# Performance work log

Hardware: AMD Instinct MI355X
Metric: run time of the kernel (lower is better)

## Reference

```python
import jax, jax.numpy as jnp
import numpy as np

N = 64      # SSM state size (hidden_size)
H = 1024    # channels
L = 2048    # sequence length
BATCH = 8


def setup_inputs() -> dict:
    key = jax.random.key(0)
    ks = jax.random.split(key, 12)
    s = 1.0 / np.sqrt(N)
    n = jnp.arange(N, dtype=jnp.float32)
    return {
        "r": jax.random.normal(ks[0], (BATCH, L, H), dtype=jnp.float32),
        "B_re": jax.random.normal(ks[1], (N,), dtype=jnp.float32) * s,
        "B_im": jax.random.normal(ks[2], (N,), dtype=jnp.float32) * s,
        "C_re": jax.random.normal(ks[3], (H, N), dtype=jnp.float32) * s,
        "C_im": jax.random.normal(ks[4], (H, N), dtype=jnp.float32) * s,
        "P_re": jax.random.normal(ks[5], (N,), dtype=jnp.float32) * s,
        "P_im": jax.random.normal(ks[6], (N,), dtype=jnp.float32) * s,
        "Q_re": jax.random.normal(ks[7], (N,), dtype=jnp.float32) * s,
        "Q_im": jax.random.normal(ks[8], (N,), dtype=jnp.float32) * s,
        # HiPPO-LegS-like diagonal: negative real part for stability, imag ~ pi*n
        "diag_re": -0.5 * jnp.ones((N,), dtype=jnp.float32),
        "diag_im": jnp.pi * (n - N / 2.0),
        "step": jnp.array([1e-3], dtype=jnp.float32),
        "D": jnp.zeros((1,), dtype=jnp.float32),
    }


def _dplr_kernel(Bc, Cc, Pc, Qc, Lam, step, seq_len):
    # Standard S4 DPLR generating function evaluated at roots of unity,
    # then inverse FFT -> real convolution kernel K_c of shape (H, L).
    z = jnp.exp(-2j * jnp.pi * jnp.arange(seq_len) / seq_len).astype(jnp.complex64)  # (L,)
    g = (2.0 / step) * (1.0 - z) / (1.0 + z)                                          # (L,)
    cden = 1.0 / (g[:, None] - Lam[None, :])                                          # (L,N) Cauchy denom
    k00 = jnp.einsum('hn,ln->hl', Cc * Bc, cden)   # (H,L)
    k01 = jnp.einsum('hn,ln->hl', Cc * Pc, cden)   # (H,L)
    k10 = jnp.einsum('n,ln->l', Qc * Bc, cden)     # (L,)
    k11 = jnp.einsum('n,ln->l', Qc * Pc, cden)     # (L,)
    at_roots = (2.0 / (1.0 + z)) * (k00 - k01 * (k10 / (1.0 + k11)))  # (H,L)
    return jnp.fft.ifft(at_roots, axis=-1).real


def reference(r, B_re, B_im, C_re, C_im, P_re, P_im, Q_re, Q_im,
              diag_re, diag_im, step, D):
    step_c = jnp.maximum(step[0], 1e-6)
    Bc = B_re + 1j * B_im
    Cc = C_re + 1j * C_im
    Pc = P_re + 1j * P_im
    Qc = Q_re + 1j * Q_im
    Lam = diag_re + 1j * diag_im
    seq_len = r.shape[1]
    K = _dplr_kernel(Bc, Cc, Pc, Qc, Lam, step_c, seq_len)  # (H, L)
    # causal FFT convolution along the sequence axis
    nfft = 2 * seq_len
    Kf = jnp.fft.rfft(K, n=nfft, axis=-1)            # (H, nfft//2+1)
    uf = jnp.fft.rfft(r, n=nfft, axis=1)             # (B, nfft//2+1, H)
    h1 = jnp.fft.irfft(uf * Kf.T[None], n=nfft, axis=1)[:, :seq_len]  # (B,L,H)
    y1 = h1 + D[0] * r
    return jax.nn.gelu(y1, approximate=False)
```

## Files before the change

### kernel.cpp

```cpp
#include <hip/hip_runtime.h>
#include <math.h>

#define SSM_N 64
#define SSM_H 1024
#define SSM_L 2048
#define SSM_B 8
#define FFTN 2048
#define NT 256

#define PSWZ(a) ((a) ^ (((a) >> 4) & 15))

typedef float f2 __attribute__((ext_vector_type(2)));
static __device__ __forceinline__ f2 mkf2(float a, float b){ f2 v; v.x = a; v.y = b; return v; }

static __device__ __forceinline__ f2 cmul(f2 a, f2 b){
  return mkf2(-a.y, a.y) * mkf2(b.y, b.x) + mkf2(a.x, a.x) * b;
}
static __device__ __forceinline__ f2 cconj(f2 a){ return mkf2(a.x, -a.y); }

template<bool INV> static __device__ __forceinline__ f2 mul_mi(f2 a){
  return INV ? mkf2(-a.y, a.x) : mkf2(a.y, -a.x);
}
template<bool INV> static __device__ __forceinline__ f2 mul_w81(f2 a){
  const float r = 0.70710678118654752440f;
  return INV ? (r * mkf2(a.x - a.y, a.y + a.x)) : (r * mkf2(a.x + a.y, a.y - a.x));
}
template<bool INV> static __device__ __forceinline__ f2 mul_w83(f2 a){
  const float r = 0.70710678118654752440f;
  return INV ? (r * mkf2(-(a.x + a.y), a.x - a.y)) : (r * mkf2(a.y - a.x, -(a.x + a.y)));
}

#define W8C0 1.f
#define W8S0 0.f
#define W8C1 0.92387953251f
#define W8S1 (-0.38268343236f)
#define W8C2 0.70710678119f
#define W8S2 (-0.70710678119f)
#define W8C3 0.38268343236f
#define W8S3 (-0.92387953251f)
#define W8C4 0.f
#define W8S4 (-1.f)
#define W8C5 (-0.38268343236f)
#define W8S5 (-0.92387953251f)
#define W8C6 (-0.70710678119f)
#define W8S6 (-0.70710678119f)
#define W8C7 (-0.92387953251f)
#define W8S7 (-0.38268343236f)

template<bool INV>
static __device__ __forceinline__ void bfly8(const f2* x, f2* y)
{
  f2 t0=x[0]+x[4], t4=x[0]-x[4];
  f2 t1=x[1]+x[5], t5=x[1]-x[5];
  f2 t2=x[2]+x[6], t6=x[2]-x[6];
  f2 t3=x[3]+x[7], t7=x[3]-x[7];
  f2 b0=t0+t2, b2=t0-t2, b1=t1+t3, b3=t1-t3;
  f2 mb3 = mul_mi<INV>(b3);
  y[0]=b0+b1; y[4]=b0-b1; y[2]=b2+mb3; y[6]=b2-mb3;
  f2 v1 = mul_w81<INV>(t5), v2 = mul_mi<INV>(t6), v3 = mul_w83<INV>(t7);
  f2 a0=t4+v2, a2=t4-v2, a1=v1+v3, a3=v1-v3;
  f2 ma3 = mul_mi<INV>(a3);
  y[1]=a0+a1; y[5]=a0-a1; y[3]=a2+ma3; y[7]=a2-ma3;
}

template<bool INV>
static __device__ __forceinline__ void calc_w8(const f2* __restrict__ tw, int j, f2* w)
{
  f2 w1 = tw[j];
  if (INV) w1.y = -w1.y;
  w[1]=w1; w[2]=cmul(w1,w1); w[3]=cmul(w[2],w1); w[4]=cmul(w[2],w[2]);
  w[5]=cmul(w[3],w[2]); w[6]=cmul(w[3],w[3]); w[7]=cmul(w[4],w[3]);
}

static __device__ __forceinline__ void twstore(f2* __restrict__ dst, const f2* y, const f2* w,
                                               int base, int S)
{
  dst[PSWZ(base)]     = y[0];
  dst[PSWZ(base+S)]   = cmul(y[1],w[1]);
  dst[PSWZ(base+2*S)] = cmul(y[2],w[2]);
  dst[PSWZ(base+3*S)] = cmul(y[3],w[3]);
  dst[PSWZ(base+4*S)] = cmul(y[4],w[4]);
  dst[PSWZ(base+5*S)] = cmul(y[5],w[5]);
  dst[PSWZ(base+6*S)] = cmul(y[6],w[6]);
  dst[PSWZ(base+7*S)] = cmul(y[7],w[7]);
}

template<bool INV>
static __device__ __forceinline__ void bfly8_store(f2* __restrict__ dst, const f2* __restrict__ tw,
                                                   f2* x, int j, int base, int S)
{
  f2 y[8]; bfly8<INV>(x, y);
  f2 w[8]; calc_w8<INV>(tw, j, w);
  twstore(dst, y, w, base, S);
}

template<bool INV, int S>
static __device__ __forceinline__ void stage8_mid(const f2* __restrict__ src, f2* __restrict__ dst,
                                                  const f2* __restrict__ tw, int t, int st)
{
  const f2* sp = src + st;
  f2 x[8];
  #pragma unroll
  for (int q = 0; q < 8; ++q) x[q] = sp[256*q];
  int i = t & (S-1);
  int j = t - i;
  bfly8_store<INV>(dst, tw, x, j, i + j*8, S);
}

template<bool INV, int S>
static __device__ __forceinline__ void stage8_mid2(const f2* __restrict__ s0, f2* __restrict__ d0,
                                                   const f2* __restrict__ s1, f2* __restrict__ d1,
                                                   const f2* __restrict__ tw, int t, int st)
{
  f2 x0[8], x1[8];
  #pragma unroll
  for (int q = 0; q < 8; ++q) x0[q] = s0[st + 256*q];
  #pragma unroll
  for (int q = 0; q < 8; ++q) x1[q] = s1[st + 256*q];
  int i = t & (S-1), j = t - i, base = i + j*8;
  f2 w[8]; calc_w8<INV>(tw, j, w);
  f2 y[8];
  bfly8<INV>(x0, y); twstore(d0, y, w, base, S);
  bfly8<INV>(x1, y); twstore(d1, y, w, base, S);
}

template<bool INV, bool HALFOUT>
static __device__ __forceinline__ void stage4f(const f2* __restrict__ src, f2* __restrict__ dst, int st)
{
  #pragma unroll
  for (int hh = 0; hh < 2; ++hh) {
    const f2* sp = src + st + 256*hh;
    f2* wp = dst + st + 256*hh;
    f2 x0=sp[0], x1=sp[512], x2=sp[1024], x3=sp[1536];
    f2 a0=x0+x2, a2=x0-x2, a1=x1+x3, a3=x1-x3;
    f2 m = mul_mi<INV>(a3);
    wp[0]   = a0+a1;
    wp[512] = a2+m;
    if (!HALFOUT) {
      wp[1024] = a0-a1;
      wp[1536] = a2-m;
    }
  }
}

template<bool INV>
static __device__ __forceinline__ void stage4f_reg(const f2* __restrict__ src, f2* out, int st)
{
  #pragma unroll
  for (int hh = 0; hh < 2; ++hh) {
    const f2* sp = src + st + 256*hh;
    f2 x0=sp[0], x1=sp[512], x2=sp[1024], x3=sp[1536];
    f2 a0=x0+x2, a2=x0-x2, a1=x1+x3, a3=x1-x3;
    f2 m = mul_mi<INV>(a3);
    out[hh]   = a0+a1;
    out[hh+2] = a2+m;
    out[hh+4] = a0-a1;
    out[hh+6] = a2-m;
  }
}

static __device__ __forceinline__ f2 init_tw(f2* tw, int t)
{
  float s, c;
  sincosf(-6.2831853071795864769f * (float)t / (float)FFTN, &s, &c);
  f2 v = mkf2(c, s);
  tw[t] = v;
  return v;
}

__global__ __launch_bounds__(256) void kprep(
    const float* __restrict__ r, float* __restrict__ rT,
    const float* __restrict__ B_re, const float* __restrict__ B_im,
    const float* __restrict__ P_re, const float* __restrict__ P_im,
    const float* __restrict__ Q_re, const float* __restrict__ Q_im,
    const float* __restrict__ diag_re, const float* __restrict__ diag_im,
    const float* __restrict__ step,
    f2* __restrict__ cdenT, f2* __restrict__ f2v, f2* __restrict__ facv)
{
  __shared__ float til[64][65];
  int bid = blockIdx.x;
  int t = threadIdx.x;
  if (bid < 4096) {
    int tx = t & 15, ty = t >> 4;
    int h0 = (bid & 15) * 64, l0 = ((bid >> 4) & 31) * 64, b = bid >> 9;
    const float4* s4 = (const float4*)(r + ((size_t)b*SSM_L + l0)*SSM_H + h0);
    #pragma unroll
    for (int i = 0; i < 4; ++i) {
      int lr = ty + 16*i;
      float4 v = s4[(size_t)lr*(SSM_H/4) + tx];
      til[lr][4*tx+0]=v.x; til[lr][4*tx+1]=v.y; til[lr][4*tx+2]=v.z; til[lr][4*tx+3]=v.w;
    }
    __syncthreads();
    float4* d4 = (float4*)(rT + ((size_t)b*SSM_H + h0)*SSM_L + l0);
    #pragma unroll
    for (int i = 0; i < 4; ++i) {
      int hr = ty + 16*i;
      float4 w;
      w.x = til[4*tx+0][hr]; w.y = til[4*tx+1][hr];
      w.z = til[4*tx+2][hr]; w.w = til[4*tx+3][hr];
      d4[(size_t)hr*(SSM_L/4) + tx] = w;
    }
  } else {
    int gid = (bid - 4096) * 256 + t;
    int l = gid >> 3, s = gid & 7;
    double stepc = (double)step[0]; if (stepc < 1e-6) stepc = 1e-6;
    double ang = -2.0 * 3.14159265358979323846 * (double)l / (double)SSM_L;
    double zr = cos(ang), zi = sin(ang);
    double dr = 1.0 + zr, di = zi;
    double nr = 1.0 - zr, ni = -zi;
    double den = dr*dr + di*di;
    double i2s = 2.0 / stepc;
    double gr = i2s * (nr*dr + ni*di) / den;
    double gi = i2s * (ni*dr - nr*di) / den;
    double k10r=0.0, k10i=0.0, k11r=0.0, k11i=0.0;
    #pragma unroll
    for (int q = 0; q < 8; ++q) {
      int n = s*8 + q;
      double ar = gr - (double)diag_re[n];
      double ai = gi - (double)diag_im[n];
      double d2 = ar*ar + ai*ai;
      double cr = ar/d2, ci = -ai/d2;
      cdenT[n*SSM_L + l] = mkf2((float)cr, (float)ci);
      double qr = (double)Q_re[n], qi = (double)Q_im[n];
      double br = (double)B_re[n], bi = (double)B_im[n];
      double pr = (double)P_re[n], pi = (double)P_im[n];
      double qbr = qr*br - qi*bi, qbi = qr*bi + qi*br;
      double qpr = qr*pr - qi*pi, qpi = qr*pi + qi*pr;
      k10r += qbr*cr - qbi*ci; k10i += qbr*ci + qbi*cr;
      k11r += qpr*cr - qpi*ci; k11i += qpr*ci + qpi*cr;
    }
    #pragma unroll
    for (int off = 1; off < 8; off <<= 1) {
      k10r += __shfl_xor(k10r, off);
      k10i += __shfl_xor(k10i, off);
      k11r += __shfl_xor(k11r, off);
      k11i += __shfl_xor(k11i, off);
    }
    if (s == 0) {
      f2v[l] = mkf2((float)(2.0*dr/den), (float)(-2.0*di/den));
      double er = 1.0 + k11r, ei = k11i;
      double ed = er*er + ei*ei;
      facv[l] = mkf2((float)((k10r*er + k10i*ei)/ed), (float)((k10i*er - k10r*ei)/ed));
    }
  }
}

__global__ __launch_bounds__(NT, 2) void kkern(
    const float* __restrict__ C_re, const float* __restrict__ C_im,
    const float* __restrict__ B_re, const float* __restrict__ B_im,
    const float* __restrict__ P_re, const float* __restrict__ P_im,
    const f2* __restrict__ cdenT, const f2* __restrict__ f2v, const f2* __restrict__ facv,
    float4* __restrict__ PQg)
{
  __shared__ f2 bufA[2][FFTN];
  __shared__ f2 bufB[2][FFTN];
  __shared__ f2 tw[256];
  int t = threadIdx.x, st = PSWZ(t);
  int h0 = blockIdx.x * 2;
  f2 u = init_tw(tw, t);
  f2* cbs = bufA[0];
  if (t < 128) {
    int h = h0 + (t >> 6), n = t & 63;
    f2 cc = mkf2(C_re[h*SSM_N + n], C_im[h*SSM_N + n]);
    cbs[t]       = cmul(cc, mkf2(B_re[n], B_im[n]));
    cbs[128 + t] = cmul(cc, mkf2(P_re[n], P_im[n]));
  }
  __syncthreads();
  f2 k00[2][8], k01[2][8];
  #pragma unroll
  for (int h = 0; h < 2; ++h)
    #pragma unroll
    for (int i = 0; i < 8; ++i) { k00[h][i] = mkf2(0.f,0.f); k01[h][i] = mkf2(0.f,0.f); }
  f2 cd[8];
  #pragma unroll
  for (int i = 0; i < 8; ++i) cd[i] = cdenT[t + i*NT];
  for (int n = 0; n < SSM_N; ++n) {
    f2 cdn[8];
    #pragma unroll
    for (int i = 0; i < 8; ++i) cdn[i] = cdenT[((n+1)&63)*SSM_L + t + i*NT];
    #pragma unroll
    for (int h = 0; h < 2; ++h) {
      f2 cb = cbs[h*64 + n], cp = cbs[128 + h*64 + n];
      #pragma unroll
      for (int i = 0; i < 8; ++i) {
        k00[h][i] = k00[h][i] + cmul(cb, cd[i]);
        k01[h][i] = k01[h][i] + cmul(cp, cd[i]);
      }
    }
    #pragma unroll
    for (int i = 0; i < 8; ++i) cd[i] = cdn[i];
  }
  float sb, cb2;
  sincosf(-3.14159265358979f * (float)t / (float)FFTN, &sb, &cb2);
  f2 cbase = mkf2(cb2, sb);
  __syncthreads();
  f2 ar[2][8];
  #pragma unroll
  for (int hh = 0; hh < 2; ++hh)
    #pragma unroll
    for (int i = 0; i < 8; ++i) {
      int l = t + i*NT;
      f2 fv = f2v[l], fc = facv[l];
      ar[hh][i] = cmul(fv, k00[hh][i] - cmul(k01[hh][i], fc));
      bufA[hh][PSWZ(l)] = ar[hh][i];
    }
  __syncthreads();
  f2 ebin[2][4], e2048[2];
  e2048[0] = mkf2(0.f,0.f); e2048[1] = mkf2(0.f,0.f);
  #pragma unroll
  for (int ch = 0; ch < 2; ++ch) {
    #pragma unroll
    for (int i = 0; i < 4; ++i) {
      int m = t + i*NT;
      if (m == 0) {
        ebin[ch][0] = mkf2(bufA[ch][0].x, 0.f);
        e2048[ch]   = mkf2(bufA[ch][PSWZ(FFTN/2)].x, 0.f);
      } else {
        ebin[ch][i] = 0.5f * (bufA[ch][PSWZ(m)] + cconj(bufA[ch][PSWZ(FFTN - m)]));
      }
    }
  }
  {
    f2 w[8]; calc_w8<true>(tw, t, w);
    f2 y[8];
    bfly8<true>(ar[0], y); twstore(bufB[0], y, w, t*8, 1);
    bfly8<true>(ar[1], y); twstore(bufB[1], y, w, t*8, 1);
  }
  __syncthreads();
  stage8_mid2<true, 8>(bufB[0], bufA[0], bufB[1], bufA[1], tw, t, st);
  __syncthreads();
  stage8_mid2<true, 64>(bufA[0], bufB[0], bufA[1], bufB[1], tw, t, st);
  __syncthreads();
  {
    f2 kr0[8], kr1[8];
    stage4f_reg<true>(bufB[0], kr0, st);
    stage4f_reg<true>(bufB[1], kr1, st);
    const float Wc8[8] = {W8C0,W8C1,W8C2,W8C3,W8C4,W8C5,W8C6,W8C7};
    const float Ws8[8] = {W8S0,W8S1,W8S2,W8S3,W8S4,W8S5,W8S6,W8S7};
    const float scale = 1.0f / (float)FFTN;
    #pragma unroll
    for (int q = 0; q < 8; ++q) {
      f2 tq = cmul(cbase, mkf2(Wc8[q], Ws8[q]));
      kr0[q] = (kr0[q].x * scale) * tq;
      kr1[q] = (kr1[q].x * scale) * tq;
    }
    f2 w[8]; calc_w8<false>(tw, t, w);
    f2 y[8];
    bfly8<false>(kr0, y); twstore(bufA[0], y, w, t*8, 1);
    bfly8<false>(kr1, y); twstore(bufA[1], y, w, t*8, 1);
  }
  __syncthreads();
  stage8_mid2<false, 8>(bufA[0], bufB[0], bufA[1], bufB[1], tw, t, st);
  __syncthreads();
  stage8_mid2<false, 64>(bufB[0], bufA[0], bufB[1], bufA[1], tw, t, st);
  __syncthreads();
  #pragma unroll
  for (int ch = 0; ch < 2; ++ch) {
    stage4f<false, true>(bufA[ch], bufB[ch], st);
    #pragma unroll
    for (int i = 0; i < 4; ++i) {
      int m = t + i*NT;
      f2 v = ebin[ch][i];
      if (m == 0) v = e2048[ch];
      bufB[ch][1024 + m] = v;
    }
  }
  __syncthreads();
  const float q4 = 1.0f / 4096.0f;
  const f2 c1 = mkf2(0.99999882345170176f, -0.00153398018628477f);
  f2 base_odd = cmul(c1, u);
  const float Wc8[8] = {W8C0,W8C1,W8C2,W8C3,W8C4,W8C5,W8C6,W8C7};
  const float Ws8[8] = {W8S0,W8S1,W8S2,W8S3,W8S4,W8S5,W8S6,W8S7};
  #pragma unroll
  for (int ch = 0; ch < 2; ++ch) {
    float4* pqrow = PQg + (size_t)(h0 + ch) * FFTN;
    #pragma unroll
    for (int i = 0; i < 4; ++i) {
      int m = t + i*NT;
      f2 Ka = ebin[ch][i];
      f2 Kb = bufB[ch][1024 + ((1024 - m) & 1023)];
      f2 ee = cmul(u, mkf2(Wc8[2*i], Ws8[2*i]));
      float cv = ee.x, sv = -ee.y;
      float am = q4*(1.f - sv), ap = q4*(1.f + sv), cq = q4*cv;
      f2 P = mkf2(Ka.x*am + Kb.x*ap, Ka.y*am - Kb.y*ap);
      f2 dd = mkf2(Ka.x - Kb.x, Ka.y + Kb.y);
      pqrow[2*m] = make_float4(P.x, P.y, -dd.y*cq, dd.x*cq);
      f2 Ko = bufB[ch][PSWZ(m)];
      f2 Kp = bufB[ch][PSWZ(1023 - m)];
      f2 eo = cmul(base_odd, mkf2(Wc8[2*i], Ws8[2*i]));
      cv = eo.x; sv = -eo.y;
      am = q4*(1.f - sv); ap = q4*(1.f + sv); cq = q4*cv;
      f2 P2 = mkf2(Ko.x*am + Kp.x*ap, Ko.y*am - Kp.y*ap);
      f2 d2 = mkf2(Ko.x - Kp.x, Ko.y + Kp.y);
      pqrow[2*m+1] = make_float4(P2.x, P2.y, -d2.y*cq, d2.x*cq);
    }
  }
}

__global__ __launch_bounds__(NT, 4) void kconv(float* __restrict__ rT,
                                               const float4* __restrict__ PQg,
                                               const float* __restrict__ Dp)
{
  __shared__ f2 bufA[FFTN];
  __shared__ f2 bufB[FFTN];
  __shared__ f2 tw[256];
  int t = threadIdx.x, st = PSWZ(t);
  int xc = blockIdx.x & 7, y = blockIdx.x >> 3;
  int h = xc * 128 + (y >> 3);
  int b = y & 7;
  float Dv = Dp[0];
  init_tw(tw, t);
  float* rrow = rT + ((size_t)b*SSM_H + h) * SSM_L;
  const f2* r2 = (const f2*)rrow;
  f2 rv[4];
  #pragma unroll
  for (int i = 0; i < 4; ++i) rv[i] = r2[t + i*NT];
  {
    f2 xx[8];
    #pragma unroll
    for (int q = 0; q < 4; ++q) { xx[q] = rv[q]; xx[q+4] = mkf2(0.f, 0.f); }
    bfly8_store<false>(bufB, tw, xx, t, t*8, 1);
  }
  __syncthreads();
  stage8_mid<false, 8>(bufB, bufA, tw, t, st);
  __syncthreads();
  stage8_mid<false, 64>(bufA, bufB, tw, t, st);
  __syncthreads();
  const float4* pqrow = PQg + (size_t)h * FFTN;
  float4 pq[8];
  #pragma unroll
  for (int i = 0; i < 8; ++i) pq[i] = pqrow[t + i*NT];
  stage4f<false, false>(bufB, bufA, st);
  __syncthreads();
  {
    f2 xx[8];
    #pragma unroll
    for (int i = 0; i < 8; ++i) {
      int k = t + i*NT;
      int kk = (FFTN - k) & (FFTN - 1);
      f2 Ck  = bufA[st + i*NT];
      f2 Ckk = bufA[PSWZ(kk)];
      xx[i] = cmul(mkf2(pq[i].x, pq[i].y), Ck) + cmul(mkf2(pq[i].z, pq[i].w), cconj(Ckk));
    }
    bfly8_store<true>(bufB, tw, xx, t, t*8, 1);
  }
  __syncthreads();
  stage8_mid<true, 8>(bufB, bufA, tw, t, st);
  __syncthreads();
  stage8_mid<true, 64>(bufA, bufB, tw, t, st);
  __syncthreads();
  f2* o2 = (f2*)rrow;
  #pragma unroll
  for (int hh = 0; hh < 2; ++hh) {
    const f2* sp = bufB + st + 256*hh;
    f2 x0=sp[0], x1=sp[512], x2=sp[1024], x3=sp[1536];
    f2 a0=x0+x2, a2=x0-x2, a1=x1+x3, a3=x1-x3;
    f2 mm = mul_mi<true>(a3);
    f2 y0 = a0+a1, y1 = a2+mm;
    f2 rA = rv[hh], rB = rv[hh+2];
    o2[t + 256*hh]       = mkf2(y0.x + Dv*rA.x, y0.y + Dv*rA.y);
    o2[t + 256*hh + 512] = mkf2(y1.x + Dv*rB.x, y1.y + Dv*rB.y);
  }
}

__global__ __launch_bounds__(256) void ktback(const float* __restrict__ yT, float* __restrict__ out)
{
  __shared__ float til[64][65];
  int t = threadIdx.x, tx = t & 15, ty = t >> 4;
  int h0 = blockIdx.x * 64, l0 = blockIdx.y * 64, b = blockIdx.z;
  const float4* s4 = (const float4*)(yT + ((size_t)b*SSM_H + h0)*SSM_L + l0);
  #pragma unroll
  for (int i = 0; i < 4; ++i) {
    int hr = ty + 16*i;
    float4 v = s4[(size_t)hr*(SSM_L/4) + tx];
    til[hr][4*tx+0]=v.x; til[hr][4*tx+1]=v.y; til[hr][4*tx+2]=v.z; til[hr][4*tx+3]=v.w;
  }
  __syncthreads();
  float4* d4 = (float4*)(out + ((size_t)b*SSM_L + l0)*SSM_H + h0);
  #pragma unroll
  for (int i = 0; i < 4; ++i) {
    int lr = ty + 16*i;
    float4 w;
    float x0 = til[4*tx+0][lr], x1 = til[4*tx+1][lr];
    float x2 = til[4*tx+2][lr], x3 = til[4*tx+3][lr];
    w.x = 0.5f * x0 * (1.0f + erff(x0 * 0.70710678118654752f));
    w.y = 0.5f * x1 * (1.0f + erff(x1 * 0.70710678118654752f));
    w.z = 0.5f * x2 * (1.0f + erff(x2 * 0.70710678118654752f));
    w.w = 0.5f * x3 * (1.0f + erff(x3 * 0.70710678118654752f));
    d4[(size_t)lr*(SSM_H/4) + tx] = w;
  }
}

extern "C" void kernel_launch(void* const* d_in, const int* in_sizes, int n_in,
                              void* d_out, int out_size, void* d_ws, size_t ws_size,
                              hipStream_t stream)
{
  const float* r       = (const float*)d_in[0];
  const float* B_re    = (const float*)d_in[1];
  const float* B_im    = (const float*)d_in[2];
  const float* C_re    = (const float*)d_in[3];
  const float* C_im    = (const float*)d_in[4];
  const float* P_re    = (const float*)d_in[5];
  const float* P_im    = (const float*)d_in[6];
  const float* Q_re    = (const float*)d_in[7];
  const float* Q_im    = (const float*)d_in[8];
  const float* diag_re = (const float*)d_in[9];
  const float* diag_im = (const float*)d_in[10];
  const float* step    = (const float*)d_in[11];
  const float* Dp      = (const float*)d_in[12];
  float* out = (float*)d_out;

  char* p = (char*)d_ws;
  float* rT  = (float*)p;  p += (size_t)SSM_B*SSM_H*SSM_L*sizeof(float);
  f2* cdenT  = (f2*)p;     p += (size_t)SSM_N*SSM_L*sizeof(f2);
  f2* f2v    = (f2*)p;     p += (size_t)SSM_L*sizeof(f2);
  f2* facv   = (f2*)p;     p += (size_t)SSM_L*sizeof(f2);
  float4* PQ = (float4*)p; p += (size_t)SSM_H*FFTN*sizeof(float4);

  kprep<<<4096 + 64, 256, 0, stream>>>(r, rT, B_re, B_im, P_re, P_im, Q_re, Q_im,
                                       diag_re, diag_im, step, cdenT, f2v, facv);
  kkern<<<SSM_H/2, NT, 0, stream>>>(C_re, C_im, B_re, B_im, P_re, P_im,
                                    cdenT, f2v, facv, PQ);
  kconv<<<SSM_B*SSM_H, NT, 0, stream>>>(rT, PQ, Dp);
  ktback<<<dim3(SSM_H/64, SSM_L/64, SSM_B), 256, 0, stream>>>(rT, out);
}
```

Measured before the change: 265.3 us.

## Halve kconv shared memory with in-place FFT stages; widen kkern to 512 threads

kconv now runs its FFT stages in place on one shared buffer. Each stage reads into registers, syncs, then writes back, which halves LDS per block and lets launch bounds ask for 8 blocks per CU. kkern moves to 512 threads, with each half-block handling one channel's FFTs instead of one thread doing both, which cuts per-thread registers and adds parallelism. The cost is an extra barrier per in-place stage in kconv.

```diff
diff --git a/kernel.cpp b/kernel.cpp
--- a/kernel.cpp
+++ b/kernel.cpp
@@ -7,6 +7,7 @@
 #define SSM_B 8
 #define FFTN 2048
 #define NT 256
+#define NT2 512
 
 #define PSWZ(a) ((a) ^ (((a) >> 4) & 15))
 
@@ -94,6 +95,22 @@
   twstore(dst, y, w, base, S);
 }
 
+template<bool INV, bool ZTOP>
+static __device__ __forceinline__ void stage8_first(const f2* __restrict__ src, f2* __restrict__ dst,
+                                                    const f2* __restrict__ tw, int t, int st)
+{
+  const f2* sp = src + st;
+  f2 x[8];
+  if (ZTOP) {
+    #pragma unroll
+    for (int q = 0; q < 4; ++q) { x[q] = sp[256*q]; x[q+4] = mkf2(0.f, 0.f); }
+  } else {
+    #pragma unroll
+    for (int q = 0; q < 8; ++q) x[q] = sp[256*q];
+  }
+  bfly8_store<INV>(dst, tw, x, t, t*8, 1);
+}
+
 template<bool INV, int S>
 static __device__ __forceinline__ void stage8_mid(const f2* __restrict__ src, f2* __restrict__ dst,
                                                   const f2* __restrict__ tw, int t, int st)
@@ -108,20 +125,17 @@
 }
 
 template<bool INV, int S>
-static __device__ __forceinline__ void stage8_mid2(const f2* __restrict__ s0, f2* __restrict__ d0,
-                                                   const f2* __restrict__ s1, f2* __restrict__ d1,
-                                                   const f2* __restrict__ tw, int t, int st)
-{
-  f2 x0[8], x1[8];
-  #pragma unroll
-  for (int q = 0; q < 8; ++q) x0[q] = s0[st + 256*q];
-  #pragma unroll
-  for (int q = 0; q < 8; ++q) x1[q] = s1[st + 256*q];
-  int i = t & (S-1), j = t - i, base = i + j*8;
-  f2 w[8]; calc_w8<INV>(tw, j, w);
-  f2 y[8];
-  bfly8<INV>(x0, y); twstore(d0, y, w, base, S);
-  bfly8<INV>(x1, y); twstore(d1, y, w, base, S);
+static __device__ __forceinline__ void stage8_mid_ip(f2* __restrict__ buf, const f2* __restrict__ tw,
+                                                     int t, int st)
+{
+  f2 x[8];
+  #pragma unroll
+  for (int q = 0; q < 8; ++q) x[q] = buf[st + 256*q];
+  __syncthreads();
+  int i = t & (S-1);
+  int j = t - i;
+  bfly8_store<INV>(buf, tw, x, j, i + j*8, S);
+  __syncthreads();
 }
 
 template<bool INV, bool HALFOUT>
@@ -141,6 +155,30 @@
       wp[1536] = a2-m;
     }
   }
+}
+
+template<bool INV>
+static __device__ __forceinline__ void stage4f_ip(f2* __restrict__ buf, int st)
+{
+  f2 xr[2][4];
+  #pragma unroll
+  for (int hh = 0; hh < 2; ++hh) {
+    const f2* sp = buf + st + 256*hh;
+    xr[hh][0]=sp[0]; xr[hh][1]=sp[512]; xr[hh][2]=sp[1024]; xr[hh][3]=sp[1536];
+  }
+  __syncthreads();
+  #pragma unroll
+  for (int hh = 0; hh < 2; ++hh) {
+    f2* wp = buf + st + 256*hh;
+    f2 a0=xr[hh][0]+xr[hh][2], a2=xr[hh][0]-xr[hh][2];
+    f2 a1=xr[hh][1]+xr[hh][3], a3=xr[hh][1]-xr[hh][3];
+    f2 m = mul_mi<INV>(a3);
+    wp[0]    = a0+a1;
+    wp[512]  = a2+m;
+    wp[1024] = a0-a1;
+    wp[1536] = a2-m;
+  }
+  __syncthreads();
 }
 
 template<bool INV>
@@ -245,7 +283,7 @@
   }
 }
 
-__global__ __launch_bounds__(NT, 2) void kkern(
+__global__ __launch_bounds__(NT2, 4) void kkern(
     const float* __restrict__ C_re, const float* __restrict__ C_im,
     const float* __restrict__ B_re, const float* __restrict__ B_im,
     const float* __restrict__ P_re, const float* __restrict__ P_im,
@@ -255,9 +293,10 @@
   __shared__ f2 bufA[2][FFTN];
   __shared__ f2 bufB[2][FFTN];
   __shared__ f2 tw[256];
-  int t = threadIdx.x, st = PSWZ(t);
+  int t = threadIdx.x;
+  int tt = t & 255, ch = t >> 8, stt = PSWZ(tt);
   int h0 = blockIdx.x * 2;
-  f2 u = init_tw(tw, t);
+  if (t < 256) init_tw(tw, t);
   f2* cbs = bufA[0];
   if (t < 128) {
     int h = h0 + (t >> 6), n = t & 63;
@@ -266,143 +305,124 @@
     cbs[128 + t] = cmul(cc, mkf2(P_re[n], P_im[n]));
   }
   __syncthreads();
-  f2 k00[2][8], k01[2][8];
-  #pragma unroll
-  for (int h = 0; h < 2; ++h)
-    #pragma unroll
-    for (int i = 0; i < 8; ++i) { k00[h][i] = mkf2(0.f,0.f); k01[h][i] = mkf2(0.f,0.f); }
-  f2 cd[8];
-  #pragma unroll
-  for (int i = 0; i < 8; ++i) cd[i] = cdenT[t + i*NT];
+  f2 k00[2][4], k01[2][4];
+  #pragma unroll
+  for (int h2 = 0; h2 < 2; ++h2)
+    #pragma unroll
+    for (int i = 0; i < 4; ++i) { k00[h2][i] = mkf2(0.f,0.f); k01[h2][i] = mkf2(0.f,0.f); }
+  f2 cd[4];
+  #pragma unroll
+  for (int i = 0; i < 4; ++i) cd[i] = cdenT[t + i*NT2];
   for (int n = 0; n < SSM_N; ++n) {
-    f2 cdn[8];
-    #pragma unroll
-    for (int i = 0; i < 8; ++i) cdn[i] = cdenT[((n+1)&63)*SSM_L + t + i*NT];
-    #pragma unroll
-    for (int h = 0; h < 2; ++h) {
-      f2 cb = cbs[h*64 + n], cp = cbs[128 + h*64 + n];
+    f2 cdn[4];
+    #pragma unroll
+    for (int i = 0; i < 4; ++i) cdn[i] = cdenT[((n+1)&63)*SSM_L + t + i*NT2];
+    #pragma unroll
+    for (int h2 = 0; h2 < 2; ++h2) {
+      f2 cb = cbs[h2*64 + n], cp = cbs[128 + h2*64 + n];
       #pragma unroll
-      for (int i = 0; i < 8; ++i) {
-        k00[h][i] = k00[h][i] + cmul(cb, cd[i]);
-        k01[h][i] = k01[h][i] + cmul(cp, cd[i]);
+      for (int i = 0; i < 4; ++i) {
+        k00[h2][i] = k00[h2][i] + cmul(cb, cd[i]);
+        k01[h2][i] = k01[h2][i] + cmul(cp, cd[i]);
       }
     }
     #pragma unroll
-    for (int i = 0; i < 8; ++i) cd[i] = cdn[i];
-  }
-  float sb, cb2;
-  sincosf(-3.14159265358979f * (float)t / (float)FFTN, &sb, &cb2);
-  f2 cbase = mkf2(cb2, sb);
-  __syncthreads();
-  f2 ar[2][8];
-  #pragma unroll
-  for (int hh = 0; hh < 2; ++hh)
-    #pragma unroll
-    for (int i = 0; i < 8; ++i) {
-      int l = t + i*NT;
+    for (int i = 0; i < 4; ++i) cd[i] = cdn[i];
+  }
+  __syncthreads();
+  #pragma unroll
+  for (int h2 = 0; h2 < 2; ++h2)
+    #pragma unroll
+    for (int i = 0; i < 4; ++i) {
+      int l = t + i*NT2;
       f2 fv = f2v[l], fc = facv[l];
-      ar[hh][i] = cmul(fv, k00[hh][i] - cmul(k01[hh][i], fc));
-      bufA[hh][PSWZ(l)] = ar[hh][i];
-    }
-  __syncthreads();
-  f2 ebin[2][4], e2048[2];
-  e2048[0] = mkf2(0.f,0.f); e2048[1] = mkf2(0.f,0.f);
-  #pragma unroll
-  for (int ch = 0; ch < 2; ++ch) {
-    #pragma unroll
-    for (int i = 0; i < 4; ++i) {
-      int m = t + i*NT;
-      if (m == 0) {
-        ebin[ch][0] = mkf2(bufA[ch][0].x, 0.f);
-        e2048[ch]   = mkf2(bufA[ch][PSWZ(FFTN/2)].x, 0.f);
-      } else {
-        ebin[ch][i] = 0.5f * (bufA[ch][PSWZ(m)] + cconj(bufA[ch][PSWZ(FFTN - m)]));
-      }
-    }
-  }
+      bufA[h2][PSWZ(l)] = cmul(fv, k00[h2][i] - cmul(k01[h2][i], fc));
+    }
+  __syncthreads();
+  f2* A  = bufA[ch];
+  f2* Bb = bufB[ch];
+  f2 ebin[4], e2048 = mkf2(0.f, 0.f);
+  #pragma unroll
+  for (int i = 0; i < 4; ++i) {
+    int m = tt + i*256;
+    if (m == 0) {
+      ebin[0] = mkf2(A[0].x, 0.f);
+      e2048   = mkf2(A[PSWZ(FFTN/2)].x, 0.f);
+    } else {
+      ebin[i] = 0.5f * (A[PSWZ(m)] + cconj(A[PSWZ(FFTN - m)]));
+    }
+  }
+  stage8_first<true, false>(A, Bb, tw, tt, stt);
+  __syncthreads();
+  stage8_mid<true, 8>(Bb, A, tw, tt, stt);
+  __syncthreads();
+  stage8_mid<true, 64>(A, Bb, tw, tt, stt);
+  __syncthreads();
   {
-    f2 w[8]; calc_w8<true>(tw, t, w);
-    f2 y[8];
-    bfly8<true>(ar[0], y); twstore(bufB[0], y, w, t*8, 1);
-    bfly8<true>(ar[1], y); twstore(bufB[1], y, w, t*8, 1);
-  }
-  __syncthreads();
-  stage8_mid2<true, 8>(bufB[0], bufA[0], bufB[1], bufA[1], tw, t, st);
-  __syncthreads();
-  stage8_mid2<true, 64>(bufA[0], bufB[0], bufA[1], bufB[1], tw, t, st);
-  __syncthreads();
-  {
-    f2 kr0[8], kr1[8];
-    stage4f_reg<true>(bufB[0], kr0, st);
-    stage4f_reg<true>(bufB[1], kr1, st);
+    f2 kr[8];
+    stage4f_reg<true>(Bb, kr, stt);
+    float sbb, cbb;
+    sincosf(-3.14159265358979f * (float)tt / (float)FFTN, &sbb, &cbb);
+    f2 cbase = mkf2(cbb, sbb);
     const float Wc8[8] = {W8C0,W8C1,W8C2,W8C3,W8C4,W8C5,W8C6,W8C7};
     const float Ws8[8] = {W8S0,W8S1,W8S2,W8S3,W8S4,W8S5,W8S6,W8S7};
     const float scale = 1.0f / (float)FFTN;
     #pragma unroll
     for (int q = 0; q < 8; ++q) {
       f2 tq = cmul(cbase, mkf2(Wc8[q], Ws8[q]));
-      kr0[q] = (kr0[q].x * scale) * tq;
-      kr1[q] = (kr1[q].x * scale) * tq;
-    }
-    f2 w[8]; calc_w8<false>(tw, t, w);
-    f2 y[8];
-    bfly8<false>(kr0, y); twstore(bufA[0], y, w, t*8, 1);
-    bfly8<false>(kr1, y); twstore(bufA[1], y, w, t*8, 1);
-  }
-  __syncthreads();
-  stage8_mid2<false, 8>(bufA[0], bufB[0], bufA[1], bufB[1], tw, t, st);
-  __syncthreads();
-  stage8_mid2<false, 64>(bufB[0], bufA[0], bufB[1], bufA[1], tw, t, st);
-  __syncthreads();
-  #pragma unroll
-  for (int ch = 0; ch < 2; ++ch) {
-    stage4f<false, true>(bufA[ch], bufB[ch], st);
-    #pragma unroll
-    for (int i = 0; i < 4; ++i) {
-      int m = t + i*NT;
-      f2 v = ebin[ch][i];
-      if (m == 0) v = e2048[ch];
-      bufB[ch][1024 + m] = v;
-    }
-  }
-  __syncthreads();
+      kr[q] = (kr[q].x * scale) * tq;
+    }
+    f2 w[8]; calc_w8<false>(tw, tt, w);
+    f2 y[8]; bfly8<false>(kr, y); twstore(A, y, w, tt*8, 1);
+  }
+  __syncthreads();
+  stage8_mid<false, 8>(A, Bb, tw, tt, stt);
+  __syncthreads();
+  stage8_mid<false, 64>(Bb, A, tw, tt, stt);
+  __syncthreads();
+  stage4f<false, true>(A, Bb, stt);
+  #pragma unroll
+  for (int i = 0; i < 4; ++i) {
+    int m = tt + 256*i;
+    f2 v = ebin[i];
+    if (m == 0) v = e2048;
+    Bb[1024 + m] = v;
+  }
+  __syncthreads();
+  f2 u = tw[tt];
   const float q4 = 1.0f / 4096.0f;
   const f2 c1 = mkf2(0.99999882345170176f, -0.00153398018628477f);
   f2 base_odd = cmul(c1, u);
   const float Wc8[8] = {W8C0,W8C1,W8C2,W8C3,W8C4,W8C5,W8C6,W8C7};
   const float Ws8[8] = {W8S0,W8S1,W8S2,W8S3,W8S4,W8S5,W8S6,W8S7};
-  #pragma unroll
-  for (int ch = 0; ch < 2; ++ch) {
-    float4* pqrow = PQg + (size_t)(h0 + ch) * FFTN;
-    #pragma unroll
-    for (int i = 0; i < 4; ++i) {
-      int m = t + i*NT;
-      f2 Ka = ebin[ch][i];
-      f2 Kb = bufB[ch][1024 + ((1024 - m) & 1023)];
-      f2 ee = cmul(u, mkf2(Wc8[2*i], Ws8[2*i]));
-      float cv = ee.x, sv = -ee.y;
-      float am = q4*(1.f - sv), ap = q4*(1.f + sv), cq = q4*cv;
-      f2 P = mkf2(Ka.x*am + Kb.x*ap, Ka.y*am - Kb.y*ap);
-      f2 dd = mkf2(Ka.x - Kb.x, Ka.y + Kb.y);
-      pqrow[2*m] = make_float4(P.x, P.y, -dd.y*cq, dd.x*cq);
-      f2 Ko = bufB[ch][PSWZ(m)];
-      f2 Kp = bufB[ch][PSWZ(1023 - m)];
-      f2 eo = cmul(base_odd, mkf2(Wc8[2*i], Ws8[2*i]));
-      cv = eo.x; sv = -eo.y;
-      am = q4*(1.f - sv); ap = q4*(1.f + sv); cq = q4*cv;
-      f2 P2 = mkf2(Ko.x*am + Kp.x*ap, Ko.y*am - Kp.y*ap);
-      f2 d2 = mkf2(Ko.x - Kp.x, Ko.y + Kp.y);
-      pqrow[2*m+1] = make_float4(P2.x, P2.y, -d2.y*cq, d2.x*cq);
-    }
-  }
-}
-
-__global__ __launch_bounds__(NT, 4) void kconv(float* __restrict__ rT,
+  float4* pqrow = PQg + (size_t)(h0 + ch) * FFTN;
+  #pragma unroll
+  for (int i = 0; i < 4; ++i) {
+    int m = tt + 256*i;
+    f2 Ka = ebin[i];
+    f2 Kb = Bb[1024 + ((1024 - m) & 1023)];
+    f2 ee = cmul(u, mkf2(Wc8[2*i], Ws8[2*i]));
+    float cv = ee.x, sv = -ee.y;
+    float am = q4*(1.f - sv), ap = q4*(1.f + sv), cq = q4*cv;
+    f2 P = mkf2(Ka.x*am + Kb.x*ap, Ka.y*am - Kb.y*ap);
+    f2 dd = mkf2(Ka.x - Kb.x, Ka.y + Kb.y);
+    pqrow[2*m] = make_float4(P.x, P.y, -dd.y*cq, dd.x*cq);
+    f2 Ko = Bb[PSWZ(m)];
+    f2 Kp = Bb[PSWZ(1023 - m)];
+    f2 eo = cmul(base_odd, mkf2(Wc8[2*i], Ws8[2*i]));
+    cv = eo.x; sv = -eo.y;
+    am = q4*(1.f - sv); ap = q4*(1.f + sv); cq = q4*cv;
+    f2 P2 = mkf2(Ko.x*am + Kp.x*ap, Ko.y*am - Kp.y*ap);
+    f2 d2 = mkf2(Ko.x - Kp.x, Ko.y + Kp.y);
+    pqrow[2*m+1] = make_float4(P2.x, P2.y, -d2.y*cq, d2.x*cq);
+  }
+}
+
+__global__ __launch_bounds__(NT, 8) void kconv(float* __restrict__ rT,
                                                const float4* __restrict__ PQg,
                                                const float* __restrict__ Dp)
 {
-  __shared__ f2 bufA[FFTN];
-  __shared__ f2 bufB[FFTN];
+  __shared__ f2 buf[FFTN];
   __shared__ f2 tw[256];
   int t = threadIdx.x, st = PSWZ(t);
   int xc = blockIdx.x & 7, y = blockIdx.x >> 3;
@@ -419,40 +439,36 @@
     f2 xx[8];
     #pragma unroll
     for (int q = 0; q < 4; ++q) { xx[q] = rv[q]; xx[q+4] = mkf2(0.f, 0.f); }
-    bfly8_store<false>(bufB, tw, xx, t, t*8, 1);
-  }
-  __syncthreads();
-  stage8_mid<false, 8>(bufB, bufA, tw, t, st);
-  __syncthreads();
-  stage8_mid<false, 64>(bufA, bufB, tw, t, st);
-  __syncthreads();
+    bfly8_store<false>(buf, tw, xx, t, t*8, 1);
+  }
+  __syncthreads();
+  stage8_mid_ip<false, 8>(buf, tw, t, st);
+  stage8_mid_ip<false, 64>(buf, tw, t, st);
   const float4* pqrow = PQg + (size_t)h * FFTN;
   float4 pq[8];
   #pragma unroll
   for (int i = 0; i < 8; ++i) pq[i] = pqrow[t + i*NT];
-  stage4f<false, false>(bufB, bufA, st);
-  __syncthreads();
+  stage4f_ip<false>(buf, st);
   {
     f2 xx[8];
     #pragma unroll
     for (int i = 0; i < 8; ++i) {
       int k = t + i*NT;
       int kk = (FFTN - k) & (FFTN - 1);
-      f2 Ck  = bufA[st + i*NT];
-      f2 Ckk = bufA[PSWZ(kk)];
+      f2 Ck  = buf[st + i*NT];
+      f2 Ckk = buf[PSWZ(kk)];
       xx[i] = cmul(mkf2(pq[i].x, pq[i].y), Ck) + cmul(mkf2(pq[i].z, pq[i].w), cconj(Ckk));
     }
-    bfly8_store<true>(bufB, tw, xx, t, t*8, 1);
-  }
-  __syncthreads();
-  stage8_mid<true, 8>(bufB, bufA, tw, t, st);
-  __syncthreads();
-  stage8_mid<true, 64>(bufA, bufB, tw, t, st);
-  __syncthreads();
+    __syncthreads();
+    bfly8_store<true>(buf, tw, xx, t, t*8, 1);
+  }
+  __syncthreads();
+  stage8_mid_ip<true, 8>(buf, tw, t, st);
+  stage8_mid_ip<true, 64>(buf, tw, t, st);
   f2* o2 = (f2*)rrow;
   #pragma unroll
   for (int hh = 0; hh < 2; ++hh) {
-    const f2* sp = bufB + st + 256*hh;
+    const f2* sp = buf + st + 256*hh;
     f2 x0=sp[0], x1=sp[512], x2=sp[1024], x3=sp[1536];
     f2 a0=x0+x2, a2=x0-x2, a1=x1+x3, a3=x1-x3;
     f2 mm = mul_mi<true>(a3);
@@ -519,8 +535,8 @@
 
   kprep<<<4096 + 64, 256, 0, stream>>>(r, rT, B_re, B_im, P_re, P_im, Q_re, Q_im,
                                        diag_re, diag_im, step, cdenT, f2v, facv);
-  kkern<<<SSM_H/2, NT, 0, stream>>>(C_re, C_im, B_re, B_im, P_re, P_im,
-                                    cdenT, f2v, facv, PQ);
+  kkern<<<SSM_H/2, NT2, 0, stream>>>(C_re, C_im, B_re, B_im, P_re, P_im,
+                                     cdenT, f2v, facv, PQ);
   kconv<<<SSM_B*SSM_H, NT, 0, stream>>>(rT, PQ, Dp);
   ktback<<<dim3(SSM_H/64, SSM_L/64, SSM_B), 256, 0, stream>>>(rT, out);
 }
```

Result: slower. 309.4 us (+16.6%).
